# Kernel tuning notes

Measured on AMD Instinct MI355X. Metric: run time of the kernel, lower is better.

## Reference

```python
import jax, jax.numpy as jnp
import numpy as np

EMB, HEAD = 2048, 128

def setup_inputs() -> dict:
    key = jax.random.key(0)
    ks = jax.random.split(key, 7)
    x = jax.random.normal(ks[0], (4, 4096, EMB), dtype=jnp.float32)
    s = 1.0 / np.sqrt(EMB)
    wK = jax.random.normal(ks[1], (EMB, HEAD), dtype=jnp.float32) * s
    bK = jax.random.normal(ks[2], (HEAD,), dtype=jnp.float32) * 0.01
    wQ = jax.random.normal(ks[3], (EMB, HEAD), dtype=jnp.float32) * s
    bQ = jax.random.normal(ks[4], (HEAD,), dtype=jnp.float32) * 0.01
    wV = jax.random.normal(ks[5], (EMB, HEAD), dtype=jnp.float32) * s
    bV = jax.random.normal(ks[6], (HEAD,), dtype=jnp.float32) * 0.01
    return {"x": x, "wK": wK, "bK": bK, "wQ": wQ, "bQ": bQ, "wV": wV, "bV": bV}

def reference(x, wK, bK, wQ, bQ, wV, bV):
    B, S, E = x.shape
    K = x @ wK + bK                      # [B,S,H]
    Q = x @ wQ + bQ
    V = x @ wV + bV
    scale = 1.0 / jnp.sqrt(jnp.float32(HEAD))
    att = jnp.einsum('bqh,bkh->bqk', Q, K) * scale   # [B,S,S]
    causal = jnp.tril(jnp.ones((S, S), dtype=bool))
    att = jnp.where(causal, att, -jnp.inf)
    att = jax.nn.softmax(att, axis=-1)
    return jnp.einsum('bqk,bkh->bqh', att, V)        # [B,S,H]
```

## Files before the change

kernel.cpp:

```cpp
#include <hip/hip_runtime.h>
#include <hip/hip_bf16.h>

#define SEQ  4096
#define BATCH 4
#define EMBD 2048
#define HDIM 128

#define SCALE_LOG2E 0.12753102721944556f

typedef __bf16 bf16x8 __attribute__((ext_vector_type(8)));
typedef __bf16 bf16x4 __attribute__((ext_vector_type(4)));
typedef float  f32x4  __attribute__((ext_vector_type(4)));

__device__ __forceinline__ bf16x8 ldfrag(const __bf16* p) {
    return *(const bf16x8*)p;
}

__device__ __forceinline__ void gl_lds16(const __bf16* g, __bf16* l) {
    __builtin_amdgcn_global_load_lds(
        (const __attribute__((address_space(1))) void*)g,
        (__attribute__((address_space(3))) void*)l, 16, 0, 0);
}

__global__ __launch_bounds__(256)
void cvt_x(const float* __restrict__ x, __bf16* __restrict__ xb) {
    size_t idx = (size_t)(blockIdx.x * 256 + threadIdx.x) * 8;
    float4 v0 = *(const float4*)(x + idx);
    float4 v1 = *(const float4*)(x + idx + 4);
    bf16x8 o = { (__bf16)v0.x, (__bf16)v0.y, (__bf16)v0.z, (__bf16)v0.w,
                 (__bf16)v1.x, (__bf16)v1.y, (__bf16)v1.z, (__bf16)v1.w };
    *(bf16x8*)(xb + idx) = o;
}

__global__ __launch_bounds__(256)
void cvt_w(const float* __restrict__ wQ, const float* __restrict__ wK,
           const float* __restrict__ wV, __bf16* __restrict__ wt) {
    const float* w = (blockIdx.z == 0) ? wQ : (blockIdx.z == 1) ? wK : wV;
    __bf16* dst = wt + (size_t)blockIdx.z * HDIM * EMBD;
    int k0 = blockIdx.x * 32;
    int n0 = blockIdx.y * 32;
    __shared__ float t[32][33];
    {
        int r  = threadIdx.x >> 3;
        int c4 = (threadIdx.x & 7) * 4;
        float4 v = *(const float4*)(w + (size_t)(k0 + r) * HDIM + n0 + c4);
        t[r][c4 + 0] = v.x; t[r][c4 + 1] = v.y;
        t[r][c4 + 2] = v.z; t[r][c4 + 3] = v.w;
    }
    __syncthreads();
    {
        int n  = threadIdx.x >> 3;
        int k4 = (threadIdx.x & 7) * 4;
        bf16x4 o = { (__bf16)t[k4 + 0][n], (__bf16)t[k4 + 1][n],
                     (__bf16)t[k4 + 2][n], (__bf16)t[k4 + 3][n] };
        *(bf16x4*)(dst + (size_t)(n0 + n) * EMBD + k0 + k4) = o;
    }
}

__global__ __launch_bounds__(256, 3)
void proj(const __bf16* __restrict__ xb,
          const __bf16* __restrict__ wt,
          const float* __restrict__ bQ, const float* __restrict__ bK,
          const float* __restrict__ bV,
          __bf16* __restrict__ qws, __bf16* __restrict__ kws,
          __bf16* __restrict__ vtws) {
    const int mat  = blockIdx.y;
    const int m0   = blockIdx.x * 64;
    const int w    = threadIdx.x >> 6;
    const int lane = threadIdx.x & 63;
    const int ln   = lane & 15;
    const int quad = lane >> 4;
    const int r8   = lane >> 3;
    const int c8   = lane & 7;

    __shared__ __bf16 lA[64 * 64];
    __shared__ __bf16 lB[128 * 64];

    const __bf16* wtm = wt + (size_t)mat * (HDIM * EMBD);

    const __bf16* ga0 = xb + (size_t)(m0 + w * 16 + r8) * EMBD + (c8 ^ r8) * 8;
    const __bf16* ga1 = ga0 + (size_t)8 * EMBD;
    const __bf16* gb0 = wtm + (size_t)(w * 32 + r8) * EMBD + (c8 ^ r8) * 8;
    const __bf16* gb1 = gb0 + (size_t)8 * EMBD;
    const __bf16* gb2 = gb0 + (size_t)16 * EMBD;
    const __bf16* gb3 = gb0 + (size_t)24 * EMBD;
    __bf16* la0 = lA + (w * 16) * 64;
    __bf16* la1 = lA + (w * 16 + 8) * 64;
    __bf16* lb0 = lB + (w * 32) * 64;
    __bf16* lb1 = lB + (w * 32 + 8) * 64;
    __bf16* lb2 = lB + (w * 32 + 16) * 64;
    __bf16* lb3 = lB + (w * 32 + 24) * 64;

    const int wm0 = (w >> 1) * 32;
    const int wn0 = (w & 1) * 64;

    const f32x4 fzero = {0.f, 0.f, 0.f, 0.f};
    f32x4 acc[2][4];
#pragma unroll
    for (int i = 0; i < 2; i++)
#pragma unroll
        for (int j = 0; j < 4; j++) acc[i][j] = fzero;

    for (int k0 = 0; k0 < EMBD; k0 += 64) {
        gl_lds16(ga0 + k0, la0);
        gl_lds16(ga1 + k0, la1);
        gl_lds16(gb0 + k0, lb0);
        gl_lds16(gb1 + k0, lb1);
        gl_lds16(gb2 + k0, lb2);
        gl_lds16(gb3 + k0, lb3);
        __syncthreads();

        bf16x8 a[2][2], bb[4][2];
#pragma unroll
        for (int i = 0; i < 2; i++)
#pragma unroll
            for (int kk = 0; kk < 2; kk++)
                a[i][kk] = ldfrag(lA + (wm0 + i * 16 + ln) * 64 +
                                  (((quad + 4 * kk) ^ (ln & 7)) * 8));
#pragma unroll
        for (int j = 0; j < 4; j++)
#pragma unroll
            for (int kk = 0; kk < 2; kk++)
                bb[j][kk] = ldfrag(lB + (wn0 + j * 16 + ln) * 64 +
                                   (((quad + 4 * kk) ^ (ln & 7)) * 8));
#pragma unroll
        for (int i = 0; i < 2; i++)
#pragma unroll
            for (int j = 0; j < 4; j++)
#pragma unroll
                for (int kk = 0; kk < 2; kk++)
                    acc[i][j] = __builtin_amdgcn_mfma_f32_16x16x32_bf16(
                        a[i][kk], bb[j][kk], acc[i][j], 0, 0, 0);
        __syncthreads();
    }

    const float* bias = (mat == 0) ? bQ : (mat == 1) ? bK : bV;
#pragma unroll
    for (int j = 0; j < 4; j++) {
        int col = wn0 + j * 16 + ln;
        float bv = bias[col];
#pragma unroll
        for (int i = 0; i < 2; i++) {
            int rowb = m0 + wm0 + i * 16 + quad * 4;
            if (mat == 2) {
                int bb_ = rowb >> 12;
                int s   = rowb & (SEQ - 1);
                bf16x4 pack = { (__bf16)(acc[i][j][0] + bv),
                                (__bf16)(acc[i][j][1] + bv),
                                (__bf16)(acc[i][j][2] + bv),
                                (__bf16)(acc[i][j][3] + bv) };
                *(bf16x4*)(vtws + ((size_t)bb_ * HDIM + col) * SEQ + s) = pack;
            } else {
                __bf16* dst = (mat == 0) ? qws : kws;
#pragma unroll
                for (int r = 0; r < 4; r++)
                    dst[(size_t)(rowb + r) * HDIM + col] =
                        (__bf16)(acc[i][j][r] + bv);
            }
        }
    }
}

__global__ __launch_bounds__(256)
void attn(const __bf16* __restrict__ qws, const __bf16* __restrict__ kws,
          const __bf16* __restrict__ vtws, float* __restrict__ out) {
    const int b    = blockIdx.x & 3;
    const int qt   = (SEQ / 64 - 1) - (blockIdx.x >> 2);
    const int q0   = qt * 64;
    const int w    = threadIdx.x >> 6;
    const int lane = threadIdx.x & 63;
    const int ln   = lane & 15;
    const int quad = lane >> 4;

    __shared__ __bf16 lK[2][64 * 128];
    __shared__ __bf16 lV[2][128 * 64];
    __shared__ __bf16 lP[4][16 * 72];

    const __bf16* kws_b = kws + (size_t)b * SEQ * HDIM;
    const __bf16* vt_b  = vtws + (size_t)b * HDIM * SEQ;

    const __bf16* qbase =
        qws + ((size_t)(b * SEQ) + q0 + w * 16 + ln) * HDIM + quad * 8;
    bf16x8 qf[4];
#pragma unroll
    for (int kk = 0; kk < 4; kk++) qf[kk] = ldfrag(qbase + kk * 32);

    const f32x4 fzero = {0.f, 0.f, 0.f, 0.f};
    float lrun[4];
    f32x4 oacc[8];
#pragma unroll
    for (int r = 0; r < 4; r++) lrun[r] = 0.f;
#pragma unroll
    for (int j = 0; j < 8; j++) oacc[j] = fzero;

    const int krow_i = lane >> 4;
    const int kslot  = lane & 15;
    const int vrow_i = lane >> 3;
    const int vslot  = lane & 7;

    auto stageK = [&](int k0, int buf) {
#pragma unroll
        for (int i = 0; i < 4; i++) {
            int row = w * 16 + i * 4 + krow_i;
            const __bf16* src = kws_b + (size_t)(k0 + row) * HDIM +
                                ((kslot ^ (row & 7)) * 8);
            gl_lds16(src, &lK[buf][(w * 16 + i * 4) * 128]);
        }
    };
    auto stageV = [&](int k0, int buf) {
#pragma unroll
        for (int i = 0; i < 4; i++) {
            int row = w * 32 + i * 8 + vrow_i;
            const __bf16* src = vt_b + (size_t)row * SEQ + k0 +
                                ((vslot ^ (row & 7)) * 8);
            gl_lds16(src, &lV[buf][(w * 32 + i * 8) * 64]);
        }
    };

    const int ktiles = qt + 1;
    stageK(0, 0);
    stageV(0, 0);

    for (int kt = 0; kt < ktiles; kt++) {
        __syncthreads();
        const int cur = kt & 1;
        if (kt + 1 < ktiles) {
            stageK((kt + 1) * 64, cur ^ 1);
            stageV((kt + 1) * 64, cur ^ 1);
        }

        f32x4 sacc[4];
#pragma unroll
        for (int j = 0; j < 4; j++) sacc[j] = fzero;
        const __bf16* Kb = lK[cur];
#pragma unroll
        for (int j = 0; j < 4; j++) {
#pragma unroll
            for (int kk = 0; kk < 4; kk++) {
                bf16x8 kf = ldfrag(Kb + (j * 16 + ln) * 128 +
                                   (((quad + 4 * kk) ^ (ln & 7)) * 8));
                sacc[j] = __builtin_amdgcn_mfma_f32_16x16x32_bf16(
                    qf[kk], kf, sacc[j], 0, 0, 0);
            }
        }

        const bool diag = (kt == qt);
#pragma unroll
        for (int j = 0; j < 4; j++) {
#pragma unroll
            for (int r = 0; r < 4; r++) {
                float p = exp2f(sacc[j][r] * SCALE_LOG2E);
                if (diag) {
                    int col = kt * 64 + j * 16 + ln;
                    int row = q0 + w * 16 + quad * 4 + r;
                    if (col > row) p = 0.f;
                }
                lrun[r] += p;
                lP[w][(quad * 4 + r) * 72 + j * 16 + ln] = (__bf16)p;
            }
        }

        __builtin_amdgcn_s_waitcnt(0xc07f);
        bf16x8 af0 = ldfrag(&lP[w][ln * 72 + quad * 8]);
        bf16x8 af1 = ldfrag(&lP[w][ln * 72 + 32 + quad * 8]);

        const __bf16* Vb = lV[cur];
#pragma unroll
        for (int j = 0; j < 8; j++) {
            bf16x8 v0 = ldfrag(Vb + (j * 16 + ln) * 64 +
                               ((quad ^ (ln & 7)) * 8));
            bf16x8 v1 = ldfrag(Vb + (j * 16 + ln) * 64 +
                               (((quad + 4) ^ (ln & 7)) * 8));
            oacc[j] = __builtin_amdgcn_mfma_f32_16x16x32_bf16(
                af0, v0, oacc[j], 0, 0, 0);
            oacc[j] = __builtin_amdgcn_mfma_f32_16x16x32_bf16(
                af1, v1, oacc[j], 0, 0, 0);
        }
    }

#pragma unroll
    for (int r = 0; r < 4; r++) {
#pragma unroll
        for (int off = 8; off >= 1; off >>= 1)
            lrun[r] += __shfl_xor(lrun[r], off);
    }
#pragma unroll
    for (int r = 0; r < 4; r++) {
        float inv = 1.f / lrun[r];
        int row = q0 + w * 16 + quad * 4 + r;
        float* orow = out + ((size_t)(b * SEQ) + row) * HDIM;
#pragma unroll
        for (int j = 0; j < 8; j++) orow[j * 16 + ln] = oacc[j][r] * inv;
    }
}

extern "C" void kernel_launch(void* const* d_in, const int* in_sizes, int n_in,
                              void* d_out, int out_size, void* d_ws,
                              size_t ws_size, hipStream_t stream) {
    const float* x  = (const float*)d_in[0];
    const float* wK = (const float*)d_in[1];
    const float* bK = (const float*)d_in[2];
    const float* wQ = (const float*)d_in[3];
    const float* bQ = (const float*)d_in[4];
    const float* wV = (const float*)d_in[5];
    const float* bV = (const float*)d_in[6];
    float* out = (float*)d_out;

    __bf16* xb   = (__bf16*)d_ws;
    __bf16* wt   = xb + (size_t)BATCH * SEQ * EMBD;
    __bf16* qws  = wt + (size_t)3 * HDIM * EMBD;
    __bf16* kws  = qws + (size_t)BATCH * SEQ * HDIM;
    __bf16* vtws = kws + (size_t)BATCH * SEQ * HDIM;

    hipLaunchKernelGGL(cvt_w, dim3(EMBD / 32, HDIM / 32, 3), dim3(256), 0,
                       stream, wQ, wK, wV, wt);
    hipLaunchKernelGGL(cvt_x, dim3((size_t)BATCH * SEQ * EMBD / (8 * 256)),
                       dim3(256), 0, stream, x, xb);
    hipLaunchKernelGGL(proj, dim3(SEQ * BATCH / 64, 3), dim3(256), 0, stream,
                       xb, wt, bQ, bK, bV, qws, kws, vtws);
    hipLaunchKernelGGL(attn, dim3(BATCH * (SEQ / 64)), dim3(256), 0, stream,
                       qws, kws, vtws, out);
}
```

Baseline: 340.5 us.

## Split attention KV range across blocks and split-K the QKV projection

The causal attention kernel now splits each query tile's key range into chunks of up to 8 key tiles, giving 1152 similarly sized work items. It writes unnormalised partial outputs and row sums, which a new attn_fin kernel adds up and normalises. The projection GEMM now uses 128-row tiles and splits the embedding dimension in two, writing bf16 partials that a new qkv_fin kernel sums, adds bias to and transposes for V. The aim is to fix the load imbalance of causal attention and raise parallelism. The cost is extra partial-buffer traffic, two more launches, and bf16 rounding of the projection partials.

```diff
diff --git a/kernel.cpp b/kernel.cpp
--- a/kernel.cpp
+++ b/kernel.cpp
@@ -1,5 +1,6 @@
 #include <hip/hip_runtime.h>
 #include <hip/hip_bf16.h>
+#include <math.h>
 
 #define SEQ  4096
 #define BATCH 4
@@ -60,114 +61,141 @@
 __global__ __launch_bounds__(256, 3)
 void proj(const __bf16* __restrict__ xb,
           const __bf16* __restrict__ wt,
-          const float* __restrict__ bQ, const float* __restrict__ bK,
-          const float* __restrict__ bV,
-          __bf16* __restrict__ qws, __bf16* __restrict__ kws,
-          __bf16* __restrict__ vtws) {
+          __bf16* __restrict__ pout) {
     const int mat  = blockIdx.y;
-    const int m0   = blockIdx.x * 64;
-    const int w    = threadIdx.x >> 6;
+    const int z    = blockIdx.z;
+    const int m0   = blockIdx.x * 128;
+    const int kb   = z * (EMBD / 2);
+    const int wv   = threadIdx.x >> 6;
     const int lane = threadIdx.x & 63;
     const int ln   = lane & 15;
     const int quad = lane >> 4;
     const int r8   = lane >> 3;
     const int c8   = lane & 7;
 
-    __shared__ __bf16 lA[64 * 64];
+    __shared__ __bf16 lA[128 * 64];
     __shared__ __bf16 lB[128 * 64];
 
     const __bf16* wtm = wt + (size_t)mat * (HDIM * EMBD);
-
-    const __bf16* ga0 = xb + (size_t)(m0 + w * 16 + r8) * EMBD + (c8 ^ r8) * 8;
-    const __bf16* ga1 = ga0 + (size_t)8 * EMBD;
-    const __bf16* gb0 = wtm + (size_t)(w * 32 + r8) * EMBD + (c8 ^ r8) * 8;
-    const __bf16* gb1 = gb0 + (size_t)8 * EMBD;
-    const __bf16* gb2 = gb0 + (size_t)16 * EMBD;
-    const __bf16* gb3 = gb0 + (size_t)24 * EMBD;
-    __bf16* la0 = lA + (w * 16) * 64;
-    __bf16* la1 = lA + (w * 16 + 8) * 64;
-    __bf16* lb0 = lB + (w * 32) * 64;
-    __bf16* lb1 = lB + (w * 32 + 8) * 64;
-    __bf16* lb2 = lB + (w * 32 + 16) * 64;
-    __bf16* lb3 = lB + (w * 32 + 24) * 64;
-
-    const int wm0 = (w >> 1) * 32;
-    const int wn0 = (w & 1) * 64;
+    const __bf16* gaS = xb  + (size_t)(m0 + wv * 32 + r8) * EMBD + kb + (c8 ^ r8) * 8;
+    const __bf16* gbS = wtm + (size_t)(wv * 32 + r8) * EMBD + kb + (c8 ^ r8) * 8;
+    __bf16* laD = lA + (wv * 32) * 64;
+    __bf16* lbD = lB + (wv * 32) * 64;
+
+    const int wm0 = (wv >> 1) * 64;
+    const int wn0 = (wv & 1) * 64;
 
     const f32x4 fzero = {0.f, 0.f, 0.f, 0.f};
-    f32x4 acc[2][4];
-#pragma unroll
-    for (int i = 0; i < 2; i++)
+    f32x4 acc[4][4];
+#pragma unroll
+    for (int i = 0; i < 4; i++)
 #pragma unroll
         for (int j = 0; j < 4; j++) acc[i][j] = fzero;
 
-    for (int k0 = 0; k0 < EMBD; k0 += 64) {
-        gl_lds16(ga0 + k0, la0);
-        gl_lds16(ga1 + k0, la1);
-        gl_lds16(gb0 + k0, lb0);
-        gl_lds16(gb1 + k0, lb1);
-        gl_lds16(gb2 + k0, lb2);
-        gl_lds16(gb3 + k0, lb3);
+    for (int k0 = 0; k0 < EMBD / 2; k0 += 64) {
+#pragma unroll
+        for (int i = 0; i < 4; i++) {
+            gl_lds16(gaS + (size_t)i * 8 * EMBD + k0, laD + i * 8 * 64);
+            gl_lds16(gbS + (size_t)i * 8 * EMBD + k0, lbD + i * 8 * 64);
+        }
         __syncthreads();
-
-        bf16x8 a[2][2], bb[4][2];
-#pragma unroll
-        for (int i = 0; i < 2; i++)
-#pragma unroll
-            for (int kk = 0; kk < 2; kk++)
-                a[i][kk] = ldfrag(lA + (wm0 + i * 16 + ln) * 64 +
-                                  (((quad + 4 * kk) ^ (ln & 7)) * 8));
-#pragma unroll
-        for (int j = 0; j < 4; j++)
-#pragma unroll
-            for (int kk = 0; kk < 2; kk++)
-                bb[j][kk] = ldfrag(lB + (wn0 + j * 16 + ln) * 64 +
-                                   (((quad + 4 * kk) ^ (ln & 7)) * 8));
-#pragma unroll
-        for (int i = 0; i < 2; i++)
+#pragma unroll
+        for (int kk = 0; kk < 2; kk++) {
+            bf16x8 a[4], bb[4];
+#pragma unroll
+            for (int i = 0; i < 4; i++)
+                a[i] = ldfrag(lA + (wm0 + i * 16 + ln) * 64 +
+                              (((quad + 4 * kk) ^ (ln & 7)) * 8));
 #pragma unroll
             for (int j = 0; j < 4; j++)
-#pragma unroll
-                for (int kk = 0; kk < 2; kk++)
+                bb[j] = ldfrag(lB + (wn0 + j * 16 + ln) * 64 +
+                               (((quad + 4 * kk) ^ (ln & 7)) * 8));
+#pragma unroll
+            for (int i = 0; i < 4; i++)
+#pragma unroll
+                for (int j = 0; j < 4; j++)
                     acc[i][j] = __builtin_amdgcn_mfma_f32_16x16x32_bf16(
-                        a[i][kk], bb[j][kk], acc[i][j], 0, 0, 0);
+                        a[i], bb[j], acc[i][j], 0, 0, 0);
+        }
         __syncthreads();
     }
 
-    const float* bias = (mat == 0) ? bQ : (mat == 1) ? bK : bV;
+    __bf16* pp = pout + (size_t)(mat * 2 + z) * 16384 * 128;
 #pragma unroll
     for (int j = 0; j < 4; j++) {
         int col = wn0 + j * 16 + ln;
-        float bv = bias[col];
-#pragma unroll
-        for (int i = 0; i < 2; i++) {
+#pragma unroll
+        for (int i = 0; i < 4; i++) {
             int rowb = m0 + wm0 + i * 16 + quad * 4;
-            if (mat == 2) {
-                int bb_ = rowb >> 12;
-                int s   = rowb & (SEQ - 1);
-                bf16x4 pack = { (__bf16)(acc[i][j][0] + bv),
-                                (__bf16)(acc[i][j][1] + bv),
-                                (__bf16)(acc[i][j][2] + bv),
-                                (__bf16)(acc[i][j][3] + bv) };
-                *(bf16x4*)(vtws + ((size_t)bb_ * HDIM + col) * SEQ + s) = pack;
-            } else {
-                __bf16* dst = (mat == 0) ? qws : kws;
-#pragma unroll
-                for (int r = 0; r < 4; r++)
-                    dst[(size_t)(rowb + r) * HDIM + col] =
-                        (__bf16)(acc[i][j][r] + bv);
-            }
+#pragma unroll
+            for (int r = 0; r < 4; r++)
+                pp[(size_t)(rowb + r) * 128 + col] = (__bf16)acc[i][j][r];
         }
     }
 }
 
 __global__ __launch_bounds__(256)
+void qkv_fin(const __bf16* __restrict__ pout,
+             const float* __restrict__ bQ, const float* __restrict__ bK,
+             const float* __restrict__ bV,
+             __bf16* __restrict__ qws, __bf16* __restrict__ kws,
+             __bf16* __restrict__ vtws) {
+    const int mat = blockIdx.y;
+    const int r0  = blockIdx.x * 16;
+    const int t   = threadIdx.x;
+    const int rl  = t >> 4;
+    const int cc  = (t & 15) * 8;
+    const float* bias = (mat == 0) ? bQ : (mat == 1) ? bK : bV;
+
+    bf16x8 p0 = *(const bf16x8*)(pout +
+        ((size_t)(mat * 2 + 0) * 16384 + r0 + rl) * 128 + cc);
+    bf16x8 p1 = *(const bf16x8*)(pout +
+        ((size_t)(mat * 2 + 1) * 16384 + r0 + rl) * 128 + cc);
+    float s[8];
+#pragma unroll
+    for (int i = 0; i < 8; i++)
+        s[i] = (float)p0[i] + (float)p1[i] + bias[cc + i];
+
+    if (mat < 2) {
+        __bf16* dst = (mat == 0) ? qws : kws;
+        bf16x8 o;
+#pragma unroll
+        for (int i = 0; i < 8; i++) o[i] = (__bf16)s[i];
+        *(bf16x8*)(dst + (size_t)(r0 + rl) * 128 + cc) = o;
+    } else {
+        __shared__ float sm[16][132];
+#pragma unroll
+        for (int i = 0; i < 8; i++) sm[rl][cc + i] = s[i];
+        __syncthreads();
+        int col = t >> 1, sg = (t & 1) * 8;
+        int bb = r0 >> 12, s0 = r0 & (SEQ - 1);
+        bf16x8 o;
+#pragma unroll
+        for (int i = 0; i < 8; i++) o[i] = (__bf16)sm[sg + i][col];
+        *(bf16x8*)(vtws + ((size_t)bb * HDIM + col) * SEQ + s0 + sg) = o;
+    }
+}
+
+__global__ __launch_bounds__(256, 2)
 void attn(const __bf16* __restrict__ qws, const __bf16* __restrict__ kws,
-          const __bf16* __restrict__ vtws, float* __restrict__ out) {
-    const int b    = blockIdx.x & 3;
-    const int qt   = (SEQ / 64 - 1) - (blockIdx.x >> 2);
-    const int q0   = qt * 64;
-    const int w    = threadIdx.x >> 6;
+          const __bf16* __restrict__ vtws,
+          float* __restrict__ Opart, float* __restrict__ Lpart) {
+    const int blk = blockIdx.x;
+    const int b   = (blk & 7) >> 1;
+    int wi = ((blk >> 3) << 1) | (blk & 1);
+    wi = 287 - wi;
+    int a = (int)((sqrtf((float)wi + 1.0f) - 1.0f) * 0.5f);
+    while (4 * (a + 1) * (a + 2) <= wi) a++;
+    while (a > 0 && 4 * a * (a + 1) > wi) a--;
+    const int rem = wi - 4 * a * (a + 1);
+    const int qt  = a * 8 + rem / (a + 1);
+    const int c   = rem - (rem / (a + 1)) * (a + 1);
+    const int q0  = qt * 64;
+    const int kt0 = c * 8;
+    const int kt1 = (kt0 + 8 < qt + 1) ? (kt0 + 8) : (qt + 1);
+    const int slot = b * 288 + wi;
+
+    const int wv   = threadIdx.x >> 6;
     const int lane = threadIdx.x & 63;
     const int ln   = lane & 15;
     const int quad = lane >> 4;
@@ -180,7 +208,7 @@
     const __bf16* vt_b  = vtws + (size_t)b * HDIM * SEQ;
 
     const __bf16* qbase =
-        qws + ((size_t)(b * SEQ) + q0 + w * 16 + ln) * HDIM + quad * 8;
+        qws + ((size_t)(b * SEQ) + q0 + wv * 16 + ln) * HDIM + quad * 8;
     bf16x8 qf[4];
 #pragma unroll
     for (int kk = 0; kk < 4; kk++) qf[kk] = ldfrag(qbase + kk * 32);
@@ -193,38 +221,35 @@
 #pragma unroll
     for (int j = 0; j < 8; j++) oacc[j] = fzero;
 
-    const int krow_i = lane >> 4;
-    const int kslot  = lane & 15;
-    const int vrow_i = lane >> 3;
-    const int vslot  = lane & 7;
+    const int krow_i = lane >> 4, kslot = lane & 15;
+    const int vrow_i = lane >> 3, vslot = lane & 7;
 
     auto stageK = [&](int k0, int buf) {
 #pragma unroll
         for (int i = 0; i < 4; i++) {
-            int row = w * 16 + i * 4 + krow_i;
+            int row = wv * 16 + i * 4 + krow_i;
             const __bf16* src = kws_b + (size_t)(k0 + row) * HDIM +
                                 ((kslot ^ (row & 7)) * 8);
-            gl_lds16(src, &lK[buf][(w * 16 + i * 4) * 128]);
+            gl_lds16(src, &lK[buf][(wv * 16 + i * 4) * 128]);
         }
     };
     auto stageV = [&](int k0, int buf) {
 #pragma unroll
         for (int i = 0; i < 4; i++) {
-            int row = w * 32 + i * 8 + vrow_i;
+            int row = wv * 32 + i * 8 + vrow_i;
             const __bf16* src = vt_b + (size_t)row * SEQ + k0 +
                                 ((vslot ^ (row & 7)) * 8);
-            gl_lds16(src, &lV[buf][(w * 32 + i * 8) * 64]);
+            gl_lds16(src, &lV[buf][(wv * 32 + i * 8) * 64]);
         }
     };
 
-    const int ktiles = qt + 1;
-    stageK(0, 0);
-    stageV(0, 0);
-
-    for (int kt = 0; kt < ktiles; kt++) {
+    stageK(kt0 * 64, 0);
+    stageV(kt0 * 64, 0);
+
+    for (int kt = kt0; kt < kt1; kt++) {
         __syncthreads();
-        const int cur = kt & 1;
-        if (kt + 1 < ktiles) {
+        const int cur = (kt - kt0) & 1;
+        if (kt + 1 < kt1) {
             stageK((kt + 1) * 64, cur ^ 1);
             stageV((kt + 1) * 64, cur ^ 1);
         }
@@ -252,17 +277,17 @@
                 float p = exp2f(sacc[j][r] * SCALE_LOG2E);
                 if (diag) {
                     int col = kt * 64 + j * 16 + ln;
-                    int row = q0 + w * 16 + quad * 4 + r;
+                    int row = q0 + wv * 16 + quad * 4 + r;
                     if (col > row) p = 0.f;
                 }
                 lrun[r] += p;
-                lP[w][(quad * 4 + r) * 72 + j * 16 + ln] = (__bf16)p;
+                lP[wv][(quad * 4 + r) * 72 + j * 16 + ln] = (__bf16)p;
             }
         }
 
         __builtin_amdgcn_s_waitcnt(0xc07f);
-        bf16x8 af0 = ldfrag(&lP[w][ln * 72 + quad * 8]);
-        bf16x8 af1 = ldfrag(&lP[w][ln * 72 + 32 + quad * 8]);
+        bf16x8 af0 = ldfrag(&lP[wv][ln * 72 + quad * 8]);
+        bf16x8 af1 = ldfrag(&lP[wv][ln * 72 + 32 + quad * 8]);
 
         const __bf16* Vb = lV[cur];
 #pragma unroll
@@ -284,14 +309,47 @@
         for (int off = 8; off >= 1; off >>= 1)
             lrun[r] += __shfl_xor(lrun[r], off);
     }
+    if (ln == 0) {
+#pragma unroll
+        for (int r = 0; r < 4; r++)
+            Lpart[(size_t)slot * 64 + wv * 16 + quad * 4 + r] = lrun[r];
+    }
+    float* Ob = Opart + (size_t)slot * 8192;
 #pragma unroll
     for (int r = 0; r < 4; r++) {
-        float inv = 1.f / lrun[r];
-        int row = q0 + w * 16 + quad * 4 + r;
-        float* orow = out + ((size_t)(b * SEQ) + row) * HDIM;
-#pragma unroll
-        for (int j = 0; j < 8; j++) orow[j * 16 + ln] = oacc[j][r] * inv;
-    }
+        int row = wv * 16 + quad * 4 + r;
+#pragma unroll
+        for (int j = 0; j < 8; j++)
+            Ob[(size_t)row * 128 + j * 16 + ln] = oacc[j][r];
+    }
+}
+
+__global__ __launch_bounds__(256)
+void attn_fin(const float* __restrict__ Opart, const float* __restrict__ Lpart,
+              float* __restrict__ out) {
+    const int b  = blockIdx.x >> 6;
+    const int qt = blockIdx.x & 63;
+    const int a  = qt >> 3;
+    const int nch = a + 1;
+    const int base = b * 288 + 4 * a * (a + 1) + (qt & 7) * (a + 1);
+    const int row = threadIdx.x >> 2;
+    const int c0  = (threadIdx.x & 3) * 32;
+
+    float l = 0.f;
+    f32x4 o[8];
+#pragma unroll
+    for (int i = 0; i < 8; i++) o[i] = {0.f, 0.f, 0.f, 0.f};
+    for (int ch = 0; ch < nch; ch++) {
+        const f32x4* Op = (const f32x4*)(Opart + (size_t)(base + ch) * 8192 +
+                                         (size_t)row * 128 + c0);
+        l += Lpart[(size_t)(base + ch) * 64 + row];
+#pragma unroll
+        for (int i = 0; i < 8; i++) o[i] += Op[i];
+    }
+    float inv = 1.f / l;
+    f32x4* orow = (f32x4*)(out + ((size_t)(b * SEQ) + qt * 64 + row) * HDIM + c0);
+#pragma unroll
+    for (int i = 0; i < 8; i++) orow[i] = o[i] * inv;
 }
 
 extern "C" void kernel_launch(void* const* d_in, const int* in_sizes, int n_in,
@@ -311,13 +369,20 @@
     __bf16* qws  = wt + (size_t)3 * HDIM * EMBD;
     __bf16* kws  = qws + (size_t)BATCH * SEQ * HDIM;
     __bf16* vtws = kws + (size_t)BATCH * SEQ * HDIM;
+    __bf16* pout = vtws + (size_t)BATCH * SEQ * HDIM;
+    float* Opart = (float*)d_ws;
+    float* Lpart = Opart + (size_t)1152 * 8192;
 
     hipLaunchKernelGGL(cvt_w, dim3(EMBD / 32, HDIM / 32, 3), dim3(256), 0,
                        stream, wQ, wK, wV, wt);
     hipLaunchKernelGGL(cvt_x, dim3((size_t)BATCH * SEQ * EMBD / (8 * 256)),
                        dim3(256), 0, stream, x, xb);
-    hipLaunchKernelGGL(proj, dim3(SEQ * BATCH / 64, 3), dim3(256), 0, stream,
-                       xb, wt, bQ, bK, bV, qws, kws, vtws);
-    hipLaunchKernelGGL(attn, dim3(BATCH * (SEQ / 64)), dim3(256), 0, stream,
-                       qws, kws, vtws, out);
-}
+    hipLaunchKernelGGL(proj, dim3(SEQ * BATCH / 128, 3, 2), dim3(256), 0,
+                       stream, xb, wt, pout);
+    hipLaunchKernelGGL(qkv_fin, dim3(SEQ * BATCH / 16, 3), dim3(256), 0,
+                       stream, pout, bQ, bK, bV, qws, kws, vtws);
+    hipLaunchKernelGGL(attn, dim3(1152), dim3(256), 0, stream,
+                       qws, kws, vtws, Opart, Lpart);
+    hipLaunchKernelGGL(attn_fin, dim3(256), dim3(256), 0, stream,
+                       Opart, Lpart, out);
+}
```

New measurement: 307.8 us. -9.6%, faster.
